# Performance work log

Measured on AMD Instinct MI355X. Metric: run time of the kernel, lower is better.

The kernel has to match this reference:

```python
import jax, jax.numpy as jnp
import numpy as np

L, H, D, HD, DFF, V, S, B = 12, 12, 768, 64, 3072, 50257, 512, 4
NEG = -1e10  # mask value used by the torch module (applied incl. diagonal, pre-scale)


def layer_norm(x, g, b, eps=1e-5):
    u = jnp.mean(x, axis=-1, keepdims=True)
    v = jnp.mean((x - u) ** 2, axis=-1, keepdims=True)  # biased variance
    return g * (x - u) / jnp.sqrt(v + eps) + b


def setup_inputs() -> dict:
    key = jax.random.key(0)
    ks = jax.random.split(key, 10)
    f = lambda k, s: 0.02 * jax.random.normal(k, s, dtype=jnp.float32)
    return {
        "tokens": jax.random.randint(ks[0], (B, S), 0, V),
        "E": f(ks[1], (V, D)),
        "P": f(ks[2], (S, D)),
        "Wq": f(ks[3], (L, H, HD, D)),
        "Wk": f(ks[4], (L, H, HD, D)),
        "Wv": f(ks[5], (L, H, HD, D)),
        "Wo": f(ks[6], (L, D, D)),
        "bo": jnp.zeros((L, D), jnp.float32),
        "g1": jnp.ones((L, D), jnp.float32),
        "b1": jnp.zeros((L, D), jnp.float32),
        "g2": jnp.ones((L, D), jnp.float32),
        "b2": jnp.zeros((L, D), jnp.float32),
        "W1": f(ks[7], (L, DFF, D)),
        "bff1": jnp.zeros((L, DFF), jnp.float32),
        "W2": f(ks[8], (L, D, DFF)),
        "bff2": jnp.zeros((L, D), jnp.float32),
        "gf": jnp.ones((D,), jnp.float32),
        "bf": jnp.zeros((D,), jnp.float32),
    }


def reference(tokens, E, P, Wq, Wk, Wv, Wo, bo, g1, b1, g2, b2, W1, bff1, W2, bff2, gf, bf):
    x = E[tokens] + P[None, :, :]  # [B,S,D]; embed_dropout is identity at eval
    # Faithful mask: triu with diagonal=0 (masks the diagonal too), added BEFORE 1/sqrt(dk)
    mask = jnp.triu(jnp.ones((S, S), jnp.float32), k=0) * NEG
    scale = 1.0 / jnp.sqrt(jnp.float32(HD))
    for l in range(L):
        h = layer_norm(x, g1[l], b1[l])
        Q = jnp.einsum('bsd,hkd->bhsk', h, Wq[l])
        K = jnp.einsum('bsd,hkd->bhsk', h, Wk[l])
        Vh = jnp.einsum('bsd,hkd->bhsk', h, Wv[l])
        sc = (jnp.einsum('bhqk,bhmk->bhqm', Q, K) + mask) * scale  # [B,H,S,S]
        A = jax.nn.softmax(sc, axis=-1)
        o = jnp.einsum('bhqm,bhmk->bhqk', A, Vh)  # [B,H,S,HD]
        o = o.transpose(0, 2, 1, 3).reshape(B, S, D)  # concat heads
        x = x + jnp.einsum('bsd,ed->bse', o, Wo[l]) + bo[l]
        h2 = layer_norm(x, g2[l], b2[l])
        ff = jax.nn.gelu(jnp.einsum('bsd,fd->bsf', h2, W1[l]) + bff1[l], approximate=False)
        x = x + jnp.einsum('bsf,df->bsd', ff, W2[l]) + bff2[l]
    x = layer_norm(x, gf, bf)
    return jnp.einsum('bsd,vd->bsv', x, E)  # weight-tied LM head
```

## Files before the change

### kernel.cpp

```cpp
#include <hip/hip_runtime.h>
#include <hip/hip_bf16.h>
#include <math.h>
#include <stdint.h>

#define L      12
#define H      12
#define DMODEL 768
#define HDIM   64
#define DFF    3072
#define VOCAB  50257
#define VPAD2  50432
#define SEQ    512
#define BATCH  4
#define MTOK   2048

typedef __hip_bfloat16 bf16;
typedef __bf16 bf16x8 __attribute__((ext_vector_type(8)));
typedef float  f32x4  __attribute__((ext_vector_type(4)));

__device__ inline float bfbits2f(unsigned int u) {
    return __builtin_bit_cast(float, u << 16);
}
__device__ inline unsigned int f2bf_bits(float f) {
    __hip_bfloat16 h = __float2bfloat16(f);
    return (unsigned int)__builtin_bit_cast(unsigned short, h);
}

typedef __attribute__((address_space(1))) unsigned int as1_uint;
typedef __attribute__((address_space(3))) unsigned int as3_uint;

__device__ inline void load_lds_16B(const void* g, void* l) {
    __builtin_amdgcn_global_load_lds((as1_uint*)(uintptr_t)g,
                                     (as3_uint*)(uintptr_t)l, 16, 0, 0);
}

__device__ inline int xcd_swz(int raw, int nwg) {
    return (raw & 7) * (nwg >> 3) + (raw >> 3);
}

__global__ void cvt_pad_kernel(bf16* __restrict__ dst, const float* __restrict__ src,
                               long ns, long nt) {
    long i8 = ((long)blockIdx.x * blockDim.x + threadIdx.x) * 8;
    long stride = (long)gridDim.x * blockDim.x * 8;
    for (; i8 < nt; i8 += stride) {
        uint4 out;
        if (i8 < ns) {
            float4 a = *reinterpret_cast<const float4*>(src + i8);
            float4 b = *reinterpret_cast<const float4*>(src + i8 + 4);
            out.x = f2bf_bits(a.x) | (f2bf_bits(a.y) << 16);
            out.y = f2bf_bits(a.z) | (f2bf_bits(a.w) << 16);
            out.z = f2bf_bits(b.x) | (f2bf_bits(b.y) << 16);
            out.w = f2bf_bits(b.z) | (f2bf_bits(b.w) << 16);
        } else {
            out = (uint4){0u, 0u, 0u, 0u};
        }
        *reinterpret_cast<uint4*>(dst + i8) = out;
    }
}

__global__ __launch_bounds__(256) void embed_ln_kernel(
        float* __restrict__ x, bf16* __restrict__ hout,
        const int* __restrict__ tok, const float* __restrict__ E,
        const float* __restrict__ P, const float* __restrict__ g,
        const float* __restrict__ b) {
    int row = blockIdx.x, tid = threadIdx.x;
    int s = row % SEQ;
    size_t ebase = (size_t)tok[row] * DMODEL;
    float v[3];
    #pragma unroll
    for (int e = 0; e < 3; e++) {
        int c = tid + e * 256;
        v[e] = E[ebase + c] + P[s * DMODEL + c];
        x[(size_t)row * DMODEL + c] = v[e];
    }
    float s1 = v[0] + v[1] + v[2];
    float s2 = v[0] * v[0] + v[1] * v[1] + v[2] * v[2];
    #pragma unroll
    for (int o = 32; o > 0; o >>= 1) {
        s1 += __shfl_down(s1, o);
        s2 += __shfl_down(s2, o);
    }
    __shared__ float w1[4], w2[4];
    int wv = tid >> 6;
    if ((tid & 63) == 0) { w1[wv] = s1; w2[wv] = s2; }
    __syncthreads();
    s1 = w1[0] + w1[1] + w1[2] + w1[3];
    s2 = w2[0] + w2[1] + w2[2] + w2[3];
    float u    = s1 * (1.f / DMODEL);
    float var  = s2 * (1.f / DMODEL) - u * u;
    float rstd = rsqrtf(var + 1e-5f);
    size_t base = (size_t)row * DMODEL;
    #pragma unroll
    for (int e = 0; e < 3; e++) {
        int c = tid + e * 256;
        hout[base + c] = __float2bfloat16(g[c] * (v[e] - u) * rstd + b[c]);
    }
}

__global__ __launch_bounds__(256) void reduce_ln_kernel(
        float* __restrict__ x, const float* __restrict__ part, int S,
        const float* __restrict__ bias, const float* __restrict__ g,
        const float* __restrict__ b, bf16* __restrict__ hout) {
    int row = blockIdx.x, tid = threadIdx.x;
    float v[3];
    #pragma unroll
    for (int e = 0; e < 3; e++) {
        int c = tid + e * 256;
        size_t idx = (size_t)row * DMODEL + c;
        float acc = x[idx] + bias[c];
        for (int s = 0; s < S; s++)
            acc += part[((size_t)s * MTOK + row) * DMODEL + c];
        v[e] = acc;
        x[idx] = acc;
    }
    float s1 = v[0] + v[1] + v[2];
    float s2 = v[0] * v[0] + v[1] * v[1] + v[2] * v[2];
    #pragma unroll
    for (int o = 32; o > 0; o >>= 1) {
        s1 += __shfl_down(s1, o);
        s2 += __shfl_down(s2, o);
    }
    __shared__ float w1[4], w2[4];
    int wv = tid >> 6;
    if ((tid & 63) == 0) { w1[wv] = s1; w2[wv] = s2; }
    __syncthreads();
    s1 = w1[0] + w1[1] + w1[2] + w1[3];
    s2 = w2[0] + w2[1] + w2[2] + w2[3];
    float u    = s1 * (1.f / DMODEL);
    float var  = s2 * (1.f / DMODEL) - u * u;
    float rstd = rsqrtf(var + 1e-5f);
    size_t base = (size_t)row * DMODEL;
    #pragma unroll
    for (int e = 0; e < 3; e++) {
        int c = tid + e * 256;
        hout[base + c] = __float2bfloat16(g[c] * (v[e] - u) * rstd + b[c]);
    }
}

#define BM 128
#define BKK 64

template<int BN_, int EPI>
__global__ __launch_bounds__(256) void gemm_bt(
    const bf16* __restrict__ A, const bf16* __restrict__ Bmat, long strideBz,
    void* __restrict__ Cout, long strideCz,
    const float* __restrict__ bias,
    int Mm, int Nn, int Kk, int Nstore, int kslice)
{
    constexpr int RING = (BN_ == 128) ? 2 : 3;
    constexpr int NF = BN_ / 32;
    constexpr int LOADS = 4 + BN_ / 32;
    __shared__ __align__(16) bf16 As[RING][BM * BKK];
    __shared__ __align__(16) bf16 Bs[RING][BN_ * BKK];
    int tid = threadIdx.x;
    int lane = tid & 63, wave = tid >> 6;

    int Mtiles = Mm / BM;
    int id = xcd_swz(blockIdx.x, gridDim.x);
    int bm = (id % Mtiles) * BM;
    int bn = (id / Mtiles) * BN_;
    int z = blockIdx.z;
    const bf16* Bz = Bmat + (size_t)z * strideBz;
    int wr = (wave >> 1) * 64, wc = (wave & 1) * (BN_ / 2);

    int k0 = (EPI == 4) ? z * kslice : 0;
    int nt = ((EPI == 4) ? kslice : Kk) / BKK;

    f32x4 acc[4][NF];
    #pragma unroll
    for (int i = 0; i < 4; i++)
        #pragma unroll
        for (int j = 0; j < NF; j++) acc[i][j] = (f32x4){0.f, 0.f, 0.f, 0.f};

    auto stage = [&](int slot, int kt) {
        #pragma unroll
        for (int i = 0; i < 4; i++) {
            int byte = i * 4096 + tid * 16;
            int r = byte >> 7;
            int scb = (byte & 127) ^ ((r & 7) << 4);
            load_lds_16B(A + (size_t)(bm + r) * Kk + kt + (scb >> 1),
                         (char*)As[slot] + byte);
        }
        #pragma unroll
        for (int i = 0; i < BN_ / 32; i++) {
            int byte = i * 4096 + tid * 16;
            int r = byte >> 7;
            int scb = (byte & 127) ^ ((r & 7) << 4);
            load_lds_16B(Bz + (size_t)(bn + r) * Kk + kt + (scb >> 1),
                         (char*)Bs[slot] + byte);
        }
    };

    const int swz_rd = (lane & 7) << 4;
    auto compute = [&](int cur) {
        #pragma unroll
        for (int kk = 0; kk < 2; ++kk) {
            bf16x8 af[4], bfr[NF];
            int ro = lane & 15;
            int cob = kk * 64 + (lane >> 4) * 16;
            #pragma unroll
            for (int mi = 0; mi < 4; mi++) {
                int row = wr + mi * 16 + ro;
                af[mi] = *reinterpret_cast<const bf16x8*>(
                    (const char*)As[cur] + row * 128 + (cob ^ swz_rd));
            }
            #pragma unroll
            for (int ni = 0; ni < NF; ni++) {
                int row = wc + ni * 16 + ro;
                bfr[ni] = *reinterpret_cast<const bf16x8*>(
                    (const char*)Bs[cur] + row * 128 + (cob ^ swz_rd));
            }
            #pragma unroll
            for (int mi = 0; mi < 4; mi++)
                #pragma unroll
                for (int ni = 0; ni < NF; ni++)
                    acc[mi][ni] = __builtin_amdgcn_mfma_f32_16x16x32_bf16(
                        af[mi], bfr[ni], acc[mi][ni], 0, 0, 0);
        }
    };

    if constexpr (RING == 3) {
        stage(0, k0);
        stage(1, k0 + BKK);
        for (int t = 0; t < nt; ++t) {
            if (t < nt - 1) {
                asm volatile("s_waitcnt vmcnt(6)" ::: "memory");
            } else {
                asm volatile("s_waitcnt vmcnt(0)" ::: "memory");
            }
            __builtin_amdgcn_s_barrier();
            __builtin_amdgcn_sched_barrier(0);
            if (t + 2 < nt) stage((t + 2) % 3, k0 + (t + 2) * BKK);
            compute(t % 3);
        }
    } else {
        stage(0, k0);
        for (int t = 0; t < nt; ++t) {
            if (t + 1 < nt) {
                stage((t + 1) & 1, k0 + (t + 1) * BKK);
                asm volatile("s_waitcnt vmcnt(8)" ::: "memory");
            } else {
                asm volatile("s_waitcnt vmcnt(0)" ::: "memory");
            }
            __builtin_amdgcn_s_barrier();
            __builtin_amdgcn_sched_barrier(0);
            compute(t & 1);
            __builtin_amdgcn_s_barrier();
        }
    }

    int rbase = bm + wr + ((lane >> 4) << 2);
    int cbase = bn + wc + (lane & 15);
    #pragma unroll
    for (int mi = 0; mi < 4; mi++) {
        #pragma unroll
        for (int ni = 0; ni < NF; ni++) {
            int col = cbase + ni * 16;
            #pragma unroll
            for (int r = 0; r < 4; r++) {
                int row = rbase + mi * 16 + r;
                float v = acc[mi][ni][r];
                if constexpr (EPI == 0) {
                    ((bf16*)Cout)[(size_t)z * strideCz + (size_t)row * Nn + col] =
                        __float2bfloat16(v);
                } else if constexpr (EPI == 2) {
                    float t = v + bias[col];
                    float gel = 0.5f * t * (1.f + erff(t * 0.70710678118654752f));
                    ((bf16*)Cout)[(size_t)row * Nn + col] = __float2bfloat16(gel);
                } else if constexpr (EPI == 3) {
                    if (col < Nstore)
                        ((float*)Cout)[(size_t)row * Nstore + col] = v;
                } else {
                    ((float*)Cout)[(size_t)z * strideCz + (size_t)row * Nn + col] = v;
                }
            }
        }
    }
}

#define NEGMASK -1e10f
#define SM_SCALE 0.125f

__global__ __launch_bounds__(256) void attn_kernel(
    bf16* __restrict__ o, const bf16* __restrict__ qb,
    const bf16* __restrict__ kb, const bf16* __restrict__ vb)
{
    __shared__ __align__(16) bf16 K_lds[64 * 64];
    __shared__ __align__(16) bf16 VT_lds[64 * 64];
    __shared__ __align__(16) bf16 P_lds[4][16 * 64];

    int tid = threadIdx.x;
    int wave = tid >> 6, lane = tid & 63;
    int g = lane >> 4;
    int cq = lane & 15;
    int idx = xcd_swz(blockIdx.x, gridDim.x);
    int qt = idx & 7;
    int bh = idx >> 3;
    int h = bh % H, b = bh / H;
    int q0 = qt * 64;
    const size_t base = ((size_t)b * SEQ) * DMODEL + h * HDIM;

    bf16x8 qa[2];
    #pragma unroll
    for (int kk = 0; kk < 2; kk++)
        qa[kk] = *reinterpret_cast<const bf16x8*>(
            qb + base + (size_t)(q0 + wave * 16 + cq) * DMODEL + kk * 32 + g * 8);

    f32x4 acc_o[4];
    #pragma unroll
    for (int df = 0; df < 4; df++) acc_o[df] = (f32x4){0.f, 0.f, 0.f, 0.f};
    float m_run[4] = {-INFINITY, -INFINITY, -INFINITY, -INFINITY};
    float l_run[4] = {0.f, 0.f, 0.f, 0.f};

    int ntiles = (qt == 0) ? (SEQ / 64) : (qt + 1);
    for (int t = 0; t < ntiles; ++t) {
        int mt = t * 64;
        __syncthreads();
        #pragma unroll
        for (int i = 0; i < 2; i++) {
            int byte = i * 4096 + tid * 16;
            int r = byte >> 7;
            int scb = (byte & 127) ^ ((r & 7) << 4);
            load_lds_16B(kb + base + (size_t)(mt + r) * DMODEL + (scb >> 1),
                         (char*)K_lds + byte);
        }
        {
            int rp = tid & 31;
            int c0 = (tid >> 5) * 8;
            const bf16* v0p = vb + base + (size_t)(mt + 2 * rp) * DMODEL + c0;
            uint4 a = *reinterpret_cast<const uint4*>(v0p);
            uint4 bb = *reinterpret_cast<const uint4*>(v0p + DMODEL);
            unsigned int au[4] = {a.x, a.y, a.z, a.w};
            unsigned int bu[4] = {bb.x, bb.y, bb.z, bb.w};
            #pragma unroll
            for (int j = 0; j < 8; j++) {
                unsigned int lo = (j & 1) ? (au[j >> 1] >> 16) : (au[j >> 1] & 0xffffu);
                unsigned int hi = (j & 1) ? (bu[j >> 1] >> 16) : (bu[j >> 1] & 0xffffu);
                int d = c0 + j;
                int byte = d * 128 + ((rp * 4) ^ ((d & 7) << 4));
                *reinterpret_cast<unsigned int*>((char*)VT_lds + byte) = lo | (hi << 16);
            }
        }
        __syncthreads();

        f32x4 s[4];
        #pragma unroll
        for (int nf = 0; nf < 4; nf++) s[nf] = (f32x4){0.f, 0.f, 0.f, 0.f};
        #pragma unroll
        for (int kk = 0; kk < 2; kk++) {
            #pragma unroll
            for (int nf = 0; nf < 4; nf++) {
                int row = nf * 16 + cq;
                bf16x8 kf = *reinterpret_cast<const bf16x8*>(
                    (const char*)K_lds + row * 128 +
                    ((kk * 64 + g * 16) ^ ((row & 7) << 4)));
                s[nf] = __builtin_amdgcn_mfma_f32_16x16x32_bf16(qa[kk], kf, s[nf], 0, 0, 0);
            }
        }

        float p[4][4];
        #pragma unroll
        for (int r = 0; r < 4; r++) {
            int qg = q0 + wave * 16 + (g << 2) + r;
            float sv[4];
            float vmax = -INFINITY;
            #pragma unroll
            for (int nf = 0; nf < 4; nf++) {
                int kv = mt + nf * 16 + cq;
                float d = s[nf][r];
                sv[nf] = (kv >= qg) ? (d + NEGMASK) * SM_SCALE : d * SM_SCALE;
                vmax = fmaxf(vmax, sv[nf]);
            }
            vmax = fmaxf(vmax, __shfl_xor(vmax, 1));
            vmax = fmaxf(vmax, __shfl_xor(vmax, 2));
            vmax = fmaxf(vmax, __shfl_xor(vmax, 4));
            vmax = fmaxf(vmax, __shfl_xor(vmax, 8));
            float nm = fmaxf(m_run[r], vmax);
            float f = __expf(m_run[r] - nm);
            m_run[r] = nm;
            float ps = 0.f;
            #pragma unroll
            for (int nf = 0; nf < 4; nf++) {
                float pv = __expf(sv[nf] - nm);
                p[nf][r] = pv;
                ps += pv;
            }
            ps += __shfl_xor(ps, 1);
            ps += __shfl_xor(ps, 2);
            ps += __shfl_xor(ps, 4);
            ps += __shfl_xor(ps, 8);
            l_run[r] = l_run[r] * f + ps;
            #pragma unroll
            for (int df = 0; df < 4; df++) acc_o[df][r] *= f;
        }

        #pragma unroll
        for (int nf = 0; nf < 4; nf++)
            #pragma unroll
            for (int r = 0; r < 4; r++) {
                int q = (g << 2) + r;
                int blog = nf * 32 + cq * 2;
                int byte = wave * 2048 + q * 128 + (blog ^ ((q & 7) << 4));
                *reinterpret_cast<unsigned short*>((char*)P_lds + byte) =
                    (unsigned short)f2bf_bits(p[nf][r]);
            }
        __syncthreads();

        #pragma unroll
        for (int kk = 0; kk < 2; kk++) {
            bf16x8 pa = *reinterpret_cast<const bf16x8*>(
                (const char*)P_lds + wave * 2048 + cq * 128 +
                ((kk * 64 + g * 16) ^ ((cq & 7) << 4)));
            #pragma unroll
            for (int df = 0; df < 4; df++) {
                int row = df * 16 + cq;
                bf16x8 vf = *reinterpret_cast<const bf16x8*>(
                    (const char*)VT_lds + row * 128 +
                    ((kk * 64 + g * 16) ^ ((row & 7) << 4)));
                acc_o[df] = __builtin_amdgcn_mfma_f32_16x16x32_bf16(pa, vf, acc_o[df], 0, 0, 0);
            }
        }
    }

    #pragma unroll
    for (int r = 0; r < 4; r++) {
        float inv = 1.f / l_run[r];
        int qg = q0 + wave * 16 + (g << 2) + r;
        #pragma unroll
        for (int df = 0; df < 4; df++) {
            o[base + (size_t)qg * DMODEL + df * 16 + cq] =
                __float2bfloat16(acc_o[df][r] * inv);
        }
    }
}

extern "C" void kernel_launch(void* const* d_in, const int* in_sizes, int n_in,
                              void* d_out, int out_size, void* d_ws, size_t ws_size,
                              hipStream_t stream)
{
    (void)in_sizes; (void)n_in; (void)out_size; (void)ws_size;
    const int*   tokens = (const int*)d_in[0];
    const float* E    = (const float*)d_in[1];
    const float* P    = (const float*)d_in[2];
    const float* Wq   = (const float*)d_in[3];
    const float* Wk   = (const float*)d_in[4];
    const float* Wv   = (const float*)d_in[5];
    const float* Wo   = (const float*)d_in[6];
    const float* bo   = (const float*)d_in[7];
    const float* g1   = (const float*)d_in[8];
    const float* b1   = (const float*)d_in[9];
    const float* g2   = (const float*)d_in[10];
    const float* b2   = (const float*)d_in[11];
    const float* W1   = (const float*)d_in[12];
    const float* bff1 = (const float*)d_in[13];
    const float* W2   = (const float*)d_in[14];
    const float* bff2 = (const float*)d_in[15];
    const float* gf   = (const float*)d_in[16];
    const float* bfin = (const float*)d_in[17];

    char* ws = (char*)d_ws;
    size_t off = 0;
    auto alloc = [&](size_t bytes) -> void* {
        void* p = ws + off;
        off += (bytes + 255) & ~(size_t)255;
        return p;
    };
    float* x     = (float*)alloc((size_t)MTOK * DMODEL * 4);
    bf16* hbuf   = (bf16*)alloc((size_t)MTOK * DMODEL * 2);
    bf16* qkv    = (bf16*)alloc((size_t)3 * MTOK * DMODEL * 2);
    bf16* obuf   = (bf16*)alloc((size_t)MTOK * DMODEL * 2);
    bf16* ffb    = (bf16*)alloc((size_t)MTOK * DFF * 2);
    float* part  = (float*)alloc((size_t)3 * MTOK * DMODEL * 4);
    bf16* Eb     = (bf16*)alloc((size_t)VPAD2 * DMODEL * 2);
    bf16* Wqkv_b = (bf16*)alloc((size_t)3 * L * DMODEL * DMODEL * 2);
    bf16* Wo_b   = (bf16*)alloc((size_t)L * DMODEL * DMODEL * 2);
    bf16* W1_b   = (bf16*)alloc((size_t)L * DFF * DMODEL * 2);
    bf16* W2_b   = (bf16*)alloc((size_t)L * DMODEL * DFF * 2);

    long nE  = (long)VOCAB * DMODEL;
    long nEp = (long)VPAD2 * DMODEL;
    cvt_pad_kernel<<<2048, 256, 0, stream>>>(Eb, E, nE, nEp);
    long nW = (long)L * DMODEL * DMODEL;
    cvt_pad_kernel<<<2048, 256, 0, stream>>>(Wqkv_b,          Wq, nW, nW);
    cvt_pad_kernel<<<2048, 256, 0, stream>>>(Wqkv_b + nW,     Wk, nW, nW);
    cvt_pad_kernel<<<2048, 256, 0, stream>>>(Wqkv_b + 2 * nW, Wv, nW, nW);
    cvt_pad_kernel<<<2048, 256, 0, stream>>>(Wo_b,            Wo, nW, nW);
    long nF = (long)L * DFF * DMODEL;
    cvt_pad_kernel<<<2048, 256, 0, stream>>>(W1_b, W1, nF, nF);
    cvt_pad_kernel<<<2048, 256, 0, stream>>>(W2_b, W2, nF, nF);

    embed_ln_kernel<<<MTOK, 256, 0, stream>>>(x, hbuf, tokens, E, P, g1, b1);

    const long pstride = (long)MTOK * DMODEL;
    for (int l = 0; l < L; ++l) {
        gemm_bt<64, 0><<<dim3(16 * 12, 1, 3), 256, 0, stream>>>(
            hbuf, Wqkv_b + (size_t)l * DMODEL * DMODEL, (long)L * DMODEL * DMODEL,
            qkv, pstride, nullptr, MTOK, DMODEL, DMODEL, 0, 0);
        attn_kernel<<<BATCH * H * (SEQ / 64), 256, 0, stream>>>(
            obuf, qkv, qkv + pstride, qkv + 2 * pstride);
        gemm_bt<64, 4><<<dim3(16 * 12, 1, 3), 256, 0, stream>>>(
            obuf, Wo_b + (size_t)l * DMODEL * DMODEL, 0,
            part, pstride, nullptr, MTOK, DMODEL, DMODEL, 0, DMODEL / 3);
        reduce_ln_kernel<<<MTOK, 256, 0, stream>>>(
            x, part, 3, bo + l * DMODEL, g2 + l * DMODEL, b2 + l * DMODEL, hbuf);
        gemm_bt<128, 2><<<dim3(16 * 24, 1, 1), 256, 0, stream>>>(
            hbuf, W1_b + (size_t)l * DFF * DMODEL, 0,
            ffb, 0, bff1 + l * DFF, MTOK, DFF, DMODEL, 0, 0);
        gemm_bt<64, 4><<<dim3(16 * 12, 1, 3), 256, 0, stream>>>(
            ffb, W2_b + (size_t)l * DMODEL * DFF, 0,
            part, pstride, nullptr, MTOK, DMODEL, DFF, 0, DFF / 3);
        const float* ng = (l < L - 1) ? (g1 + (l + 1) * DMODEL) : gf;
        const float* nb = (l < L - 1) ? (b1 + (l + 1) * DMODEL) : bfin;
        reduce_ln_kernel<<<MTOK, 256, 0, stream>>>(
            x, part, 3, bff2 + l * DMODEL, ng, nb, hbuf);
    }
    gemm_bt<128, 3><<<dim3(16 * 394, 1, 1), 256, 0, stream>>>(
        hbuf, Eb, 0, d_out, 0, nullptr, MTOK, VPAD2, DMODEL, VOCAB, 0);
}
```

Measured before the change: 1.810 ms.

## Use wave-per-row vectorized layernorm, unify GEMM double buffering, add MFMA priority hints

```diff
diff --git a/kernel.cpp b/kernel.cpp
--- a/kernel.cpp
+++ b/kernel.cpp
@@ -63,37 +63,46 @@
         const int* __restrict__ tok, const float* __restrict__ E,
         const float* __restrict__ P, const float* __restrict__ g,
         const float* __restrict__ b) {
-    int row = blockIdx.x, tid = threadIdx.x;
-    int s = row % SEQ;
-    size_t ebase = (size_t)tok[row] * DMODEL;
-    float v[3];
+    int wave = threadIdx.x >> 6, lane = threadIdx.x & 63;
+    int row = blockIdx.x * 4 + wave;
+    int s = row & (SEQ - 1);
+    long ebase = (long)tok[row] * 192;
+    const float4* E4 = (const float4*)E;
+    const float4* P4 = (const float4*)P;
+    float4 v[3];
+    float s1 = 0.f, s2 = 0.f;
     #pragma unroll
     for (int e = 0; e < 3; e++) {
-        int c = tid + e * 256;
-        v[e] = E[ebase + c] + P[s * DMODEL + c];
-        x[(size_t)row * DMODEL + c] = v[e];
-    }
-    float s1 = v[0] + v[1] + v[2];
-    float s2 = v[0] * v[0] + v[1] * v[1] + v[2] * v[2];
+        int c4 = e * 64 + lane;
+        float4 a = E4[ebase + c4];
+        float4 p = P4[s * 192 + c4];
+        a.x += p.x; a.y += p.y; a.z += p.z; a.w += p.w;
+        v[e] = a;
+        ((float4*)x)[(size_t)row * 192 + c4] = a;
+        s1 += a.x + a.y + a.z + a.w;
+        s2 += a.x * a.x + a.y * a.y + a.z * a.z + a.w * a.w;
+    }
     #pragma unroll
     for (int o = 32; o > 0; o >>= 1) {
-        s1 += __shfl_down(s1, o);
-        s2 += __shfl_down(s2, o);
-    }
-    __shared__ float w1[4], w2[4];
-    int wv = tid >> 6;
-    if ((tid & 63) == 0) { w1[wv] = s1; w2[wv] = s2; }
-    __syncthreads();
-    s1 = w1[0] + w1[1] + w1[2] + w1[3];
-    s2 = w2[0] + w2[1] + w2[2] + w2[3];
+        s1 += __shfl_xor(s1, o);
+        s2 += __shfl_xor(s2, o);
+    }
     float u    = s1 * (1.f / DMODEL);
     float var  = s2 * (1.f / DMODEL) - u * u;
     float rstd = rsqrtf(var + 1e-5f);
-    size_t base = (size_t)row * DMODEL;
     #pragma unroll
     for (int e = 0; e < 3; e++) {
-        int c = tid + e * 256;
-        hout[base + c] = __float2bfloat16(g[c] * (v[e] - u) * rstd + b[c]);
+        int c4 = e * 64 + lane;
+        float4 gg = ((const float4*)g)[c4];
+        float4 bb = ((const float4*)b)[c4];
+        float y0 = gg.x * (v[e].x - u) * rstd + bb.x;
+        float y1 = gg.y * (v[e].y - u) * rstd + bb.y;
+        float y2 = gg.z * (v[e].z - u) * rstd + bb.z;
+        float y3 = gg.w * (v[e].w - u) * rstd + bb.w;
+        uint2 o2;
+        o2.x = f2bf_bits(y0) | (f2bf_bits(y1) << 16);
+        o2.y = f2bf_bits(y2) | (f2bf_bits(y3) << 16);
+        ((uint2*)hout)[(size_t)row * 192 + c4] = o2;
     }
 }
 
@@ -101,39 +110,48 @@
         float* __restrict__ x, const float* __restrict__ part, int S,
         const float* __restrict__ bias, const float* __restrict__ g,
         const float* __restrict__ b, bf16* __restrict__ hout) {
-    int row = blockIdx.x, tid = threadIdx.x;
-    float v[3];
+    int wave = threadIdx.x >> 6, lane = threadIdx.x & 63;
+    int row = blockIdx.x * 4 + wave;
+    const float4* part4 = (const float4*)part;
+    float4 v[3];
+    float s1 = 0.f, s2 = 0.f;
     #pragma unroll
     for (int e = 0; e < 3; e++) {
-        int c = tid + e * 256;
-        size_t idx = (size_t)row * DMODEL + c;
-        float acc = x[idx] + bias[c];
-        for (int s = 0; s < S; s++)
-            acc += part[((size_t)s * MTOK + row) * DMODEL + c];
-        v[e] = acc;
-        x[idx] = acc;
-    }
-    float s1 = v[0] + v[1] + v[2];
-    float s2 = v[0] * v[0] + v[1] * v[1] + v[2] * v[2];
+        int c4 = e * 64 + lane;
+        size_t idx = (size_t)row * 192 + c4;
+        float4 a = ((const float4*)x)[idx];
+        float4 bi = ((const float4*)bias)[c4];
+        a.x += bi.x; a.y += bi.y; a.z += bi.z; a.w += bi.w;
+        for (int sl = 0; sl < S; sl++) {
+            float4 p = part4[((size_t)sl * MTOK + row) * 192 + c4];
+            a.x += p.x; a.y += p.y; a.z += p.z; a.w += p.w;
+        }
+        v[e] = a;
+        ((float4*)x)[idx] = a;
+        s1 += a.x + a.y + a.z + a.w;
+        s2 += a.x * a.x + a.y * a.y + a.z * a.z + a.w * a.w;
+    }
     #pragma unroll
     for (int o = 32; o > 0; o >>= 1) {
-        s1 += __shfl_down(s1, o);
-        s2 += __shfl_down(s2, o);
-    }
-    __shared__ float w1[4], w2[4];
-    int wv = tid >> 6;
-    if ((tid & 63) == 0) { w1[wv] = s1; w2[wv] = s2; }
-    __syncthreads();
-    s1 = w1[0] + w1[1] + w1[2] + w1[3];
-    s2 = w2[0] + w2[1] + w2[2] + w2[3];
+        s1 += __shfl_xor(s1, o);
+        s2 += __shfl_xor(s2, o);
+    }
     float u    = s1 * (1.f / DMODEL);
     float var  = s2 * (1.f / DMODEL) - u * u;
     float rstd = rsqrtf(var + 1e-5f);
-    size_t base = (size_t)row * DMODEL;
     #pragma unroll
     for (int e = 0; e < 3; e++) {
-        int c = tid + e * 256;
-        hout[base + c] = __float2bfloat16(g[c] * (v[e] - u) * rstd + b[c]);
+        int c4 = e * 64 + lane;
+        float4 gg = ((const float4*)g)[c4];
+        float4 bb = ((const float4*)b)[c4];
+        float y0 = gg.x * (v[e].x - u) * rstd + bb.x;
+        float y1 = gg.y * (v[e].y - u) * rstd + bb.y;
+        float y2 = gg.z * (v[e].z - u) * rstd + bb.z;
+        float y3 = gg.w * (v[e].w - u) * rstd + bb.w;
+        uint2 o2;
+        o2.x = f2bf_bits(y0) | (f2bf_bits(y1) << 16);
+        o2.y = f2bf_bits(y2) | (f2bf_bits(y3) << 16);
+        ((uint2*)hout)[(size_t)row * 192 + c4] = o2;
     }
 }
 
@@ -147,11 +165,9 @@
     const float* __restrict__ bias,
     int Mm, int Nn, int Kk, int Nstore, int kslice)
 {
-    constexpr int RING = (BN_ == 128) ? 2 : 3;
     constexpr int NF = BN_ / 32;
-    constexpr int LOADS = 4 + BN_ / 32;
-    __shared__ __align__(16) bf16 As[RING][BM * BKK];
-    __shared__ __align__(16) bf16 Bs[RING][BN_ * BKK];
+    __shared__ __align__(16) bf16 As[2][BM * BKK];
+    __shared__ __align__(16) bf16 Bs[2][BN_ * BKK];
     int tid = threadIdx.x;
     int lane = tid & 63, wave = tid >> 6;
 
@@ -219,34 +235,24 @@
         }
     };
 
-    if constexpr (RING == 3) {
-        stage(0, k0);
-        stage(1, k0 + BKK);
-        for (int t = 0; t < nt; ++t) {
-            if (t < nt - 1) {
-                asm volatile("s_waitcnt vmcnt(6)" ::: "memory");
-            } else {
-                asm volatile("s_waitcnt vmcnt(0)" ::: "memory");
-            }
-            __builtin_amdgcn_s_barrier();
-            __builtin_amdgcn_sched_barrier(0);
-            if (t + 2 < nt) stage((t + 2) % 3, k0 + (t + 2) * BKK);
-            compute(t % 3);
-        }
-    } else {
-        stage(0, k0);
-        for (int t = 0; t < nt; ++t) {
-            if (t + 1 < nt) {
-                stage((t + 1) & 1, k0 + (t + 1) * BKK);
+    stage(0, k0);
+    for (int t = 0; t < nt; ++t) {
+        if (t + 1 < nt) {
+            stage((t + 1) & 1, k0 + (t + 1) * BKK);
+            if constexpr (BN_ == 128) {
                 asm volatile("s_waitcnt vmcnt(8)" ::: "memory");
             } else {
-                asm volatile("s_waitcnt vmcnt(0)" ::: "memory");
-            }
-            __builtin_amdgcn_s_barrier();
-            __builtin_amdgcn_sched_barrier(0);
-            compute(t & 1);
-            __builtin_amdgcn_s_barrier();
-        }
+                asm volatile("s_waitcnt vmcnt(6)" ::: "memory");
+            }
+        } else {
+            asm volatile("s_waitcnt vmcnt(0)" ::: "memory");
+        }
+        __builtin_amdgcn_s_barrier();
+        __builtin_amdgcn_sched_barrier(0);
+        __builtin_amdgcn_s_setprio(1);
+        compute(t & 1);
+        __builtin_amdgcn_s_setprio(0);
+        __builtin_amdgcn_s_barrier();
     }
 
     int rbase = bm + wr + ((lane >> 4) << 2);
@@ -346,6 +352,7 @@
         f32x4 s[4];
         #pragma unroll
         for (int nf = 0; nf < 4; nf++) s[nf] = (f32x4){0.f, 0.f, 0.f, 0.f};
+        __builtin_amdgcn_s_setprio(1);
         #pragma unroll
         for (int kk = 0; kk < 2; kk++) {
             #pragma unroll
@@ -357,6 +364,7 @@
                 s[nf] = __builtin_amdgcn_mfma_f32_16x16x32_bf16(qa[kk], kf, s[nf], 0, 0, 0);
             }
         }
+        __builtin_amdgcn_s_setprio(0);
 
         float p[4][4];
         #pragma unroll
@@ -406,6 +414,7 @@
             }
         __syncthreads();
 
+        __builtin_amdgcn_s_setprio(1);
         #pragma unroll
         for (int kk = 0; kk < 2; kk++) {
             bf16x8 pa = *reinterpret_cast<const bf16x8*>(
@@ -420,6 +429,7 @@
                 acc_o[df] = __builtin_amdgcn_mfma_f32_16x16x32_bf16(pa, vf, acc_o[df], 0, 0, 0);
             }
         }
+        __builtin_amdgcn_s_setprio(0);
     }
 
     #pragma unroll
@@ -489,7 +499,7 @@
     cvt_pad_kernel<<<2048, 256, 0, stream>>>(W1_b, W1, nF, nF);
     cvt_pad_kernel<<<2048, 256, 0, stream>>>(W2_b, W2, nF, nF);
 
-    embed_ln_kernel<<<MTOK, 256, 0, stream>>>(x, hbuf, tokens, E, P, g1, b1);
+    embed_ln_kernel<<<MTOK / 4, 256, 0, stream>>>(x, hbuf, tokens, E, P, g1, b1);
 
     const long pstride = (long)MTOK * DMODEL;
     for (int l = 0; l < L; ++l) {
@@ -501,7 +511,7 @@
         gemm_bt<64, 4><<<dim3(16 * 12, 1, 3), 256, 0, stream>>>(
             obuf, Wo_b + (size_t)l * DMODEL * DMODEL, 0,
             part, pstride, nullptr, MTOK, DMODEL, DMODEL, 0, DMODEL / 3);
-        reduce_ln_kernel<<<MTOK, 256, 0, stream>>>(
+        reduce_ln_kernel<<<MTOK / 4, 256, 0, stream>>>(
             x, part, 3, bo + l * DMODEL, g2 + l * DMODEL, b2 + l * DMODEL, hbuf);
         gemm_bt<128, 2><<<dim3(16 * 24, 1, 1), 256, 0, stream>>>(
             hbuf, W1_b + (size_t)l * DFF * DMODEL, 0,
@@ -511,7 +521,7 @@
             part, pstride, nullptr, MTOK, DMODEL, DFF, 0, DFF / 3);
         const float* ng = (l < L - 1) ? (g1 + (l + 1) * DMODEL) : gf;
         const float* nb = (l < L - 1) ? (b1 + (l + 1) * DMODEL) : bfin;
-        reduce_ln_kernel<<<MTOK, 256, 0, stream>>>(
+        reduce_ln_kernel<<<MTOK / 4, 256, 0, stream>>>(
             x, part, 3, bff2 + l * DMODEL, ng, nb, hbuf);
     }
     gemm_bt<128, 3><<<dim3(16 * 394, 1, 1), 256, 0, stream>>>(
```

New measurement: 1.731 ms. 1.05x faster.
